# Performance work log

Hardware: AMD Instinct MI355X
Metric: run time of the kernel (lower is better)

The kernel has to match this reference:

```python
import jax, jax.numpy as jnp
import numpy as np

B, S, D, H = 2, 2048, 1024, 16
HD = D // H
NEG = -10000.0


def setup_inputs() -> dict:
    key = jax.random.key(0)
    ks = jax.random.split(key, 9)
    # xavier-uniform-like scale for square d_model x d_model weights
    lim = float(np.sqrt(6.0 / (D + D)))
    mk_w = lambda k: jax.random.uniform(k, (D, D), jnp.float32, -lim, lim)
    return {
        "q": jax.random.normal(ks[0], (B, S, D), jnp.float32),
        "k": jax.random.normal(ks[1], (B, S, D), jnp.float32),
        "v": jax.random.normal(ks[2], (B, S, D), jnp.float32),
        "attn_mask": jax.random.randint(ks[3], (B, S), 0, 2, jnp.int32),
        "Wq": mk_w(ks[4]),
        "Wk": mk_w(ks[5]),
        "Wv": mk_w(ks[6]),
        "Wo": mk_w(ks[7]),
        "mask_future": 1,
    }


def reference(q, k, v, attn_mask, Wq, Wk, Wv, Wo, mask_future):
    # nn.Linear(bias=False): y = x @ W.T
    def split_heads(x, W):
        return (x @ W.T).reshape(B, S, H, HD).transpose(0, 2, 1, 3)  # [B,H,S,HD]

    qh = split_heads(q, Wq)
    kh = split_heads(k, Wk)
    vh = split_heads(v, Wv)

    scale = 1.0 / np.sqrt(HD)
    scores = jnp.einsum("bhld,bhsd->bhls", qh, kh) * scale  # [B,H,L,S]

    if mask_future:  # static python flag
        rows = jnp.arange(S)[:, None]
        cols = jnp.arange(S)[None, :]
        causal_bias = jnp.where(cols > rows, jnp.float32(NEG), jnp.float32(0.0))
        scores = scores + causal_bias

    # masked_fill(attn_mask == 0, -10000): sets score exactly to NEG (after bias add)
    pad = attn_mask[:, None, None, :]  # [B,1,1,S]
    scores = jnp.where(pad == 0, jnp.float32(NEG), scores)

    probs = jax.nn.softmax(scores, axis=-1)
    ctx = jnp.einsum("bhls,bhsd->bhld", probs, vh)  # [B,H,L,HD]
    ctx = ctx.transpose(0, 2, 1, 3).reshape(B, S, D)
    return ctx @ Wo.T
```

## Files before the change

### kernel.cpp

```cpp
#include <hip/hip_runtime.h>
#include <hip/hip_bf16.h>

typedef __attribute__((ext_vector_type(8))) short bf16x8;
typedef __attribute__((ext_vector_type(4))) short bf16x4;
typedef __attribute__((ext_vector_type(4))) float f32x4;

#define B_ 2
#define S_ 2048
#define D_ 1024
#define H_ 16
#define HD_ 64
#define M_ 4096
#define NEGV (-10000.0f)

#if __has_builtin(__builtin_amdgcn_mfma_f32_16x16x16bf16_1k)
#define HAVE_MFMA16 1
#else
#define HAVE_MFMA16 0
#endif

static __device__ __forceinline__ unsigned short f2bf(float x) {
  __hip_bfloat16 h = __float2bfloat16(x);
  return *reinterpret_cast<unsigned short*>(&h);
}

static __device__ __forceinline__ bf16x8 cvt8(const float* p) {
  float4 a = *reinterpret_cast<const float4*>(p);
  float4 b = *reinterpret_cast<const float4*>(p + 4);
  bf16x8 r;
  r[0] = (short)f2bf(a.x); r[1] = (short)f2bf(a.y);
  r[2] = (short)f2bf(a.z); r[3] = (short)f2bf(a.w);
  r[4] = (short)f2bf(b.x); r[5] = (short)f2bf(b.y);
  r[6] = (short)f2bf(b.z); r[7] = (short)f2bf(b.w);
  return r;
}

template<bool AF32, bool BF32, bool HSPLIT>
static __device__ __forceinline__ void gemm_core(const void* Av, const void* Bv,
                                                 unsigned short* Asm, unsigned short* Bsm,
                                                 int m0, int n0, f32x4 (*acc)[4]) {
  constexpr int BK = 64, LDT = 72;
  constexpr int K = 1024;
  const int tid = threadIdx.x;
  const int lane = tid & 63, wid = tid >> 6;
  const int wm = wid >> 1, wn = wid & 1;
  const int l15 = lane & 15, l4 = lane >> 4;

  for (int k0 = 0; k0 < K; k0 += BK) {
    __syncthreads();
#pragma unroll
    for (int i = 0; i < 4; ++i) {
      int idx = tid + 256 * i;
      int row = idx >> 3, k8 = (idx & 7) * 8;
      bf16x8 va, vb;
      if constexpr (AF32) {
        va = cvt8((const float*)Av + (size_t)(m0 + row) * K + k0 + k8);
      } else if constexpr (HSPLIT) {
        const int m = m0 + row, kk = k0 + k8;
        const int bb = m >> 11, s = m & 2047;
        va = *reinterpret_cast<const bf16x8*>(
            (const unsigned short*)Av +
            (((size_t)(bb * H_ + (kk >> 6)) * S_ + s) * HD_ + (kk & 63)));
      } else {
        va = *reinterpret_cast<const bf16x8*>((const unsigned short*)Av + (size_t)(m0 + row) * K + k0 + k8);
      }
      if constexpr (BF32) {
        vb = cvt8((const float*)Bv + (size_t)(n0 + row) * K + k0 + k8);
      } else {
        vb = *reinterpret_cast<const bf16x8*>((const unsigned short*)Bv + (size_t)(n0 + row) * K + k0 + k8);
      }
      *reinterpret_cast<bf16x8*>(&Asm[row * LDT + k8]) = va;
      *reinterpret_cast<bf16x8*>(&Bsm[row * LDT + k8]) = vb;
    }
    __syncthreads();
#pragma unroll
    for (int kk = 0; kk < 2; ++kk) {
      bf16x8 af[4], bfr[4];
#pragma unroll
      for (int f = 0; f < 4; ++f) {
        af[f]  = *reinterpret_cast<const bf16x8*>(&Asm[(wm * 64 + f * 16 + l15) * LDT + kk * 32 + l4 * 8]);
        bfr[f] = *reinterpret_cast<const bf16x8*>(&Bsm[(wn * 64 + f * 16 + l15) * LDT + kk * 32 + l4 * 8]);
      }
#pragma unroll
      for (int fm = 0; fm < 4; ++fm)
#pragma unroll
        for (int fn = 0; fn < 4; ++fn)
          acc[fm][fn] = __builtin_amdgcn_mfma_f32_16x16x32_bf16(af[fm], bfr[fn], acc[fm][fn], 0, 0, 0);
    }
  }
}

__global__ __launch_bounds__(256) void gemm_qkv3(const float* __restrict__ q,
                                                 const float* __restrict__ k,
                                                 const float* __restrict__ v,
                                                 const float* __restrict__ Wq,
                                                 const float* __restrict__ Wk,
                                                 const float* __restrict__ Wv,
                                                 unsigned short* __restrict__ Qh,
                                                 unsigned short* __restrict__ Kh,
                                                 unsigned short* __restrict__ Vt) {
  constexpr int LDT = 72;
  __shared__ unsigned short Asm[128 * LDT];
  __shared__ unsigned short Bsm[128 * LDT];
  const int z = blockIdx.z;
  const float* A  = (z == 0) ? q  : (z == 1) ? k  : v;
  const float* Bw = (z == 0) ? Wq : (z == 1) ? Wk : Wv;
  const int m0 = blockIdx.y * 128, n0 = blockIdx.x * 128;
  const int lane = threadIdx.x & 63, wid = threadIdx.x >> 6;
  const int wm = wid >> 1, wn = wid & 1;
  const int l15 = lane & 15, l4 = lane >> 4;
  f32x4 acc[4][4] = {};
  gemm_core<true, true, false>(A, Bw, Asm, Bsm, m0, n0, acc);

#pragma unroll
  for (int fm = 0; fm < 4; ++fm) {
#pragma unroll
    for (int fn = 0; fn < 4; ++fn) {
      const int mg0 = m0 + wm * 64 + fm * 16 + l4 * 4;
      const int ng  = n0 + wn * 64 + fn * 16 + l15;
      const int bidx = mg0 >> 11, s = mg0 & 2047;
      const int h = ng >> 6, d = ng & 63;
      if (z < 2) {
        unsigned short* C = (z == 0) ? Qh : Kh;
#pragma unroll
        for (int r = 0; r < 4; ++r)
          C[((size_t)((bidx * H_ + h) * S_ + s + r)) * HD_ + d] = f2bf(acc[fm][fn][r]);
      } else {
        ushort4 pk;
        pk.x = f2bf(acc[fm][fn][0]); pk.y = f2bf(acc[fm][fn][1]);
        pk.z = f2bf(acc[fm][fn][2]); pk.w = f2bf(acc[fm][fn][3]);
        *reinterpret_cast<ushort4*>(&Vt[((size_t)((bidx * H_ + h) * HD_ + d)) * S_ + s]) = pk;
      }
    }
  }
}

__global__ __launch_bounds__(256) void gemm_oproj(const void* __restrict__ Av,
                                                  const void* __restrict__ Bv,
                                                  float* __restrict__ Cout) {
  constexpr int LDT = 72;
  __shared__ unsigned short Asm[128 * LDT];
  __shared__ unsigned short Bsm[128 * LDT];
  const int m0 = blockIdx.y * 128, n0 = blockIdx.x * 128;
  const int lane = threadIdx.x & 63, wid = threadIdx.x >> 6;
  const int wm = wid >> 1, wn = wid & 1;
  const int l15 = lane & 15, l4 = lane >> 4;
  f32x4 acc[4][4] = {};
  gemm_core<false, true, true>(Av, Bv, Asm, Bsm, m0, n0, acc);

#pragma unroll
  for (int fm = 0; fm < 4; ++fm)
#pragma unroll
    for (int fn = 0; fn < 4; ++fn) {
      const int mg0 = m0 + wm * 64 + fm * 16 + l4 * 4;
      const int ng  = n0 + wn * 64 + fn * 16 + l15;
#pragma unroll
      for (int r = 0; r < 4; ++r)
        Cout[(size_t)(mg0 + r) * 1024 + ng] = acc[fm][fn][r];
    }
}

__global__ __launch_bounds__(256) void attn_fwd(const unsigned short* Qh,
                                                const unsigned short* __restrict__ Kh,
                                                const unsigned short* __restrict__ Vt,
                                                const int* __restrict__ attn_mask,
                                                const int* __restrict__ mask_future,
                                                unsigned short* ctx) {
  constexpr int KVB = 128;
  constexpr int LDK = 72;
  constexpr int LDV = 136;
  __shared__ unsigned short Ksm[KVB * LDK];
  __shared__ unsigned short Vsm[64 * LDV];
#if !HAVE_MFMA16
  __shared__ unsigned short Psm[4][16 * LDV];
#endif
  __shared__ int s_any;
  const int tid = threadIdx.x, lane = tid & 63, wid = tid >> 6;
  const int l15 = lane & 15, l4 = lane >> 4;
  const int bh = blockIdx.y, b = bh >> 4;
  const int q0 = ((int)(blockIdx.x + blockIdx.y) & 31) * 64;
  const bool causal = (mask_future[0] != 0);

  if (tid == 0) s_any = 0;
  __syncthreads();
  for (int i = tid; i <= q0; i += 256)
    if (attn_mask[b * S_ + i]) s_any = 1;
  __syncthreads();
  const int kb_end = (causal && s_any) ? (q0 + 64) : S_;

  const unsigned short* Qb = Qh + (size_t)bh * S_ * HD_;
  const unsigned short* Kb = Kh + (size_t)bh * S_ * HD_;
  const unsigned short* Vb = Vt + (size_t)bh * HD_ * S_;
  const int* mrow = attn_mask + b * S_;

  const int qrow = q0 + wid * 16 + l15;
  const bf16x8 qf0 = *reinterpret_cast<const bf16x8*>(&Qb[(size_t)qrow * HD_ + l4 * 8]);
  const bf16x8 qf1 = *reinterpret_cast<const bf16x8*>(&Qb[(size_t)qrow * HD_ + 32 + l4 * 8]);

  float m_run = -1e30f, l_run = 0.f;
  f32x4 o[4] = {};

  bf16x8 kreg[4], vreg[4];
#pragma unroll
  for (int j = 0; j < 4; ++j) {
    const int idx = tid + 256 * j;
    kreg[j] = *reinterpret_cast<const bf16x8*>(&Kb[(size_t)(idx >> 3) * HD_ + (idx & 7) * 8]);
    vreg[j] = *reinterpret_cast<const bf16x8*>(&Vb[(size_t)(idx >> 4) * S_ + (idx & 15) * 8]);
  }

  for (int kb = 0; kb < kb_end; kb += KVB) {
    __syncthreads();
#pragma unroll
    for (int j = 0; j < 4; ++j) {
      const int idx = tid + 256 * j;
      *reinterpret_cast<bf16x8*>(&Ksm[(idx >> 3) * LDK + (idx & 7) * 8]) = kreg[j];
      *reinterpret_cast<bf16x8*>(&Vsm[(idx >> 4) * LDV + (idx & 15) * 8]) = vreg[j];
    }
    __syncthreads();

    if (kb + KVB < kb_end) {
      const int kn = kb + KVB;
#pragma unroll
      for (int j = 0; j < 4; ++j) {
        const int idx = tid + 256 * j;
        kreg[j] = *reinterpret_cast<const bf16x8*>(&Kb[(size_t)(kn + (idx >> 3)) * HD_ + (idx & 7) * 8]);
        vreg[j] = *reinterpret_cast<const bf16x8*>(&Vb[(size_t)(idx >> 4) * S_ + kn + (idx & 15) * 8]);
      }
    }

    f32x4 sc[8];
#pragma unroll
    for (int nf = 0; nf < 8; ++nf) {
      bf16x8 kf0 = *reinterpret_cast<const bf16x8*>(&Ksm[(nf * 16 + l15) * LDK + l4 * 8]);
      bf16x8 kf1 = *reinterpret_cast<const bf16x8*>(&Ksm[(nf * 16 + l15) * LDK + 32 + l4 * 8]);
      f32x4 z = {};
      z = __builtin_amdgcn_mfma_f32_16x16x32_bf16(kf0, qf0, z, 0, 0, 0);
      z = __builtin_amdgcn_mfma_f32_16x16x32_bf16(kf1, qf1, z, 0, 0, 0);
      sc[nf] = z;
    }

    float p[8][4];
    float mx = -1e30f;
#pragma unroll
    for (int nf = 0; nf < 8; ++nf) {
      const int4 mk4 = *reinterpret_cast<const int4*>(&mrow[kb + nf * 16 + l4 * 4]);
      const int kbase = kb + nf * 16 + l4 * 4;
#pragma unroll
      for (int r = 0; r < 4; ++r) {
        float vv = sc[nf][r] * 0.125f;
        if (causal && (kbase + r) > qrow) vv += NEGV;
        const int mkr = (r == 0) ? mk4.x : (r == 1) ? mk4.y : (r == 2) ? mk4.z : mk4.w;
        if (mkr == 0) vv = NEGV;
        p[nf][r] = vv;
        mx = fmaxf(mx, vv);
      }
    }
    mx = fmaxf(mx, __shfl_xor(mx, 16));
    mx = fmaxf(mx, __shfl_xor(mx, 32));
    const float m_new = fmaxf(m_run, mx);
    const float scale = __expf(m_run - m_new);
    float s_loc = 0.f;
#pragma unroll
    for (int nf = 0; nf < 8; ++nf)
#pragma unroll
      for (int r = 0; r < 4; ++r) {
        float e = __expf(p[nf][r] - m_new);
        p[nf][r] = e;
        s_loc += e;
      }
    s_loc += __shfl_xor(s_loc, 16);
    s_loc += __shfl_xor(s_loc, 32);
    l_run = l_run * scale + s_loc;
    m_run = m_new;

    float sq[4];
#pragma unroll
    for (int r = 0; r < 4; ++r) sq[r] = __shfl(scale, l4 * 4 + r);
#pragma unroll
    for (int nf2 = 0; nf2 < 4; ++nf2)
#pragma unroll
      for (int r = 0; r < 4; ++r) o[nf2][r] *= sq[r];

#if HAVE_MFMA16
    bf16x4 pk[8];
#pragma unroll
    for (int nf = 0; nf < 8; ++nf) {
      bf16x4 t;
      t[0] = (short)f2bf(p[nf][0]); t[1] = (short)f2bf(p[nf][1]);
      t[2] = (short)f2bf(p[nf][2]); t[3] = (short)f2bf(p[nf][3]);
      pk[nf] = t;
    }
#pragma unroll
    for (int nf2 = 0; nf2 < 4; ++nf2) {
#pragma unroll
      for (int nf = 0; nf < 8; ++nf) {
        bf16x4 vf = *reinterpret_cast<const bf16x4*>(&Vsm[(nf2 * 16 + l15) * LDV + nf * 16 + l4 * 4]);
        o[nf2] = __builtin_amdgcn_mfma_f32_16x16x16bf16_1k(pk[nf], vf, o[nf2], 0, 0, 0);
      }
    }
#else
    unsigned short* Pw = &Psm[wid][0];
#pragma unroll
    for (int nf = 0; nf < 8; ++nf)
#pragma unroll
      for (int r = 0; r < 4; ++r)
        Pw[l15 * LDV + nf * 16 + l4 * 4 + r] = f2bf(p[nf][r]);
#pragma unroll
    for (int nf2 = 0; nf2 < 4; ++nf2) {
#pragma unroll
      for (int kk = 0; kk < 4; ++kk) {
        bf16x8 pf = *reinterpret_cast<const bf16x8*>(&Pw[l15 * LDV + kk * 32 + l4 * 8]);
        bf16x8 vf = *reinterpret_cast<const bf16x8*>(&Vsm[(nf2 * 16 + l15) * LDV + kk * 32 + l4 * 8]);
        o[nf2] = __builtin_amdgcn_mfma_f32_16x16x32_bf16(pf, vf, o[nf2], 0, 0, 0);
      }
    }
#endif
  }

  const float linv = 1.f / l_run;
  float lq[4];
#pragma unroll
  for (int r = 0; r < 4; ++r) lq[r] = __shfl(linv, l4 * 4 + r);
#pragma unroll
  for (int nf2 = 0; nf2 < 4; ++nf2)
#pragma unroll
    for (int r = 0; r < 4; ++r) {
      const int rowg = q0 + wid * 16 + l4 * 4 + r;
      ctx[((size_t)bh * S_ + rowg) * HD_ + nf2 * 16 + l15] = f2bf(o[nf2][r] * lq[r]);
    }
}

extern "C" void kernel_launch(void* const* d_in, const int* in_sizes, int n_in,
                              void* d_out, int out_size, void* d_ws, size_t ws_size,
                              hipStream_t stream) {
  const float* q = (const float*)d_in[0];
  const float* k = (const float*)d_in[1];
  const float* v = (const float*)d_in[2];
  const int* attn_mask = (const int*)d_in[3];
  const float* Wq = (const float*)d_in[4];
  const float* Wk = (const float*)d_in[5];
  const float* Wv = (const float*)d_in[6];
  const float* Wo = (const float*)d_in[7];
  const int* mask_future = (const int*)d_in[8];

  const size_t n16 = (size_t)M_ * D_;
  unsigned short* ws0 = (unsigned short*)d_ws;
  unsigned short* ws1 = ws0 + n16;
  unsigned short* Vt  = (unsigned short*)d_out;
  float* out = (float*)d_out;
  (void)in_sizes; (void)n_in; (void)out_size; (void)ws_size;

  gemm_qkv3<<<dim3(8, 32, 3), 256, 0, stream>>>(q, k, v, Wq, Wk, Wv, ws0, ws1, Vt);
  attn_fwd<<<dim3(S_ / 64, B_ * H_), 256, 0, stream>>>(ws0, ws1, Vt, attn_mask, mask_future, ws0);
  gemm_oproj<<<dim3(8, 32), 256, 0, stream>>>(ws0, Wo, out);
}
```

Before: 203.0 us.

## Pre-convert inputs to bf16 and use direct-to-LDS swizzled GEMM loads

Adds a conversion kernel that turns q, k, v and all weights into bf16 once, so the projection GEMMs stop converting fp32 inside their load loops. New GEMM cores load tiles with global_load_lds into XOR-swizzled LDS and use the 16x16x32 bf16 MFMA. The attention tile order switches to an XOR-based swizzle to balance causal work across heads. The cost is an extra kernel launch and extra workspace traffic for the bf16 copies, and there is a fallback to the old path when the workspace is too small.

```diff
diff --git a/kernel.cpp b/kernel.cpp
--- a/kernel.cpp
+++ b/kernel.cpp
@@ -12,6 +12,9 @@
 #define HD_ 64
 #define M_ 4096
 #define NEGV (-10000.0f)
+
+#define NQ_ 4194304
+#define NW_ 1048576
 
 #if __has_builtin(__builtin_amdgcn_mfma_f32_16x16x16bf16_1k)
 #define HAVE_MFMA16 1
@@ -34,6 +37,155 @@
   r[6] = (short)f2bf(b.z); r[7] = (short)f2bf(b.w);
   return r;
 }
+
+static __device__ __forceinline__ void gl_lds16(const unsigned short* g, unsigned short* l) {
+#if __has_builtin(__builtin_amdgcn_global_load_lds)
+  __builtin_amdgcn_global_load_lds(
+      (const __attribute__((address_space(1))) unsigned int*)g,
+      (__attribute__((address_space(3))) unsigned int*)l, 16, 0, 0);
+#else
+  *reinterpret_cast<bf16x8*>(l) = *reinterpret_cast<const bf16x8*>(g);
+#endif
+}
+
+
+__global__ __launch_bounds__(256) void cvt_all(const float* __restrict__ q,
+                                               const float* __restrict__ k,
+                                               const float* __restrict__ v,
+                                               const float* __restrict__ wq,
+                                               const float* __restrict__ wk,
+                                               const float* __restrict__ wv,
+                                               const float* __restrict__ wo,
+                                               unsigned short* __restrict__ dst) {
+  for (size_t c = (size_t)blockIdx.x * 256 + threadIdx.x; c < 2097152; c += (size_t)2048 * 256) {
+    const size_t e = c * 8;
+    const float* s;
+    if (e < (size_t)NQ_)            s = q  + e;
+    else if (e < (size_t)2 * NQ_)   s = k  + (e - (size_t)NQ_);
+    else if (e < (size_t)3 * NQ_)   s = v  + (e - (size_t)2 * NQ_);
+    else if (e < (size_t)3 * NQ_ + NW_)     s = wq + (e - (size_t)3 * NQ_);
+    else if (e < (size_t)3 * NQ_ + 2 * NW_) s = wk + (e - (size_t)3 * NQ_ - NW_);
+    else if (e < (size_t)3 * NQ_ + 3 * NW_) s = wv + (e - (size_t)3 * NQ_ - 2 * NW_);
+    else                                    s = wo + (e - (size_t)3 * NQ_ - 3 * NW_);
+    *reinterpret_cast<bf16x8*>(dst + e) = cvt8(s);
+  }
+}
+
+template<bool HSPLIT>
+static __device__ __forceinline__ void core_fast(const unsigned short* A,
+                                                 const unsigned short* Bw,
+                                                 unsigned short* Asm, unsigned short* Bsm,
+                                                 int m0, int n0, f32x4 (*acc)[4]) {
+  const int tid = threadIdx.x, lane = tid & 63, wid = tid >> 6;
+  const int wm = wid >> 1, wn = wid & 1;
+  const int l15 = lane & 15, l4 = lane >> 4;
+
+  for (int k0 = 0; k0 < 1024; k0 += 64) {
+    __syncthreads();
+#pragma unroll
+    for (int i = 0; i < 4; ++i) {
+      const int idx = tid + 256 * i;
+      const int row = idx >> 3;
+      const int ce = ((idx & 7) * 8) ^ ((row & 7) << 3);
+      const unsigned short* ga;
+      if constexpr (HSPLIT) {
+        const int m = m0 + row, kk = k0 + ce;
+        const int bb = m >> 11, s = m & 2047;
+        ga = A + (((size_t)(bb * H_ + (kk >> 6)) * S_ + s) * HD_ + (kk & 63));
+      } else {
+        ga = A + (size_t)(m0 + row) * 1024 + k0 + ce;
+      }
+      gl_lds16(ga, Asm + (size_t)idx * 8);
+      gl_lds16(Bw + (size_t)(n0 + row) * 1024 + k0 + ce, Bsm + (size_t)idx * 8);
+    }
+    __syncthreads();
+#pragma unroll
+    for (int kk = 0; kk < 2; ++kk) {
+      bf16x8 af[4], bfr[4];
+#pragma unroll
+      for (int f = 0; f < 4; ++f) {
+        const int ra = wm * 64 + f * 16 + l15;
+        const int ca = (kk * 32 + l4 * 8) ^ ((ra & 7) << 3);
+        af[f] = *reinterpret_cast<const bf16x8*>(&Asm[ra * 64 + ca]);
+        const int rb = wn * 64 + f * 16 + l15;
+        const int cb = (kk * 32 + l4 * 8) ^ ((rb & 7) << 3);
+        bfr[f] = *reinterpret_cast<const bf16x8*>(&Bsm[rb * 64 + cb]);
+      }
+#pragma unroll
+      for (int fm = 0; fm < 4; ++fm)
+#pragma unroll
+        for (int fn = 0; fn < 4; ++fn)
+          acc[fm][fn] = __builtin_amdgcn_mfma_f32_16x16x32_bf16(af[fm], bfr[fn], acc[fm][fn], 0, 0, 0);
+    }
+  }
+}
+
+__global__ __launch_bounds__(256) void gemm_qkv_fast(const unsigned short* __restrict__ qbf,
+                                                     const unsigned short* __restrict__ kbf,
+                                                     const unsigned short* __restrict__ vbf,
+                                                     const unsigned short* __restrict__ wbf,
+                                                     unsigned short* __restrict__ Qh,
+                                                     unsigned short* __restrict__ Kh,
+                                                     unsigned short* __restrict__ Vt) {
+  __shared__ unsigned short Asm[128 * 64];
+  __shared__ unsigned short Bsm[128 * 64];
+  const int z = blockIdx.z;
+  const unsigned short* A  = (z == 0) ? qbf : (z == 1) ? kbf : vbf;
+  const unsigned short* Bw = wbf + (size_t)z * NW_;
+  const int m0 = blockIdx.y * 128, n0 = blockIdx.x * 128;
+  const int lane = threadIdx.x & 63, wid = threadIdx.x >> 6;
+  const int wm = wid >> 1, wn = wid & 1;
+  const int l15 = lane & 15, l4 = lane >> 4;
+  f32x4 acc[4][4] = {};
+  core_fast<false>(A, Bw, Asm, Bsm, m0, n0, acc);
+
+#pragma unroll
+  for (int fm = 0; fm < 4; ++fm) {
+#pragma unroll
+    for (int fn = 0; fn < 4; ++fn) {
+      const int mg0 = m0 + wm * 64 + fm * 16 + l4 * 4;
+      const int ng  = n0 + wn * 64 + fn * 16 + l15;
+      const int bidx = mg0 >> 11, s = mg0 & 2047;
+      const int h = ng >> 6, d = ng & 63;
+      if (z < 2) {
+        unsigned short* C = (z == 0) ? Qh : Kh;
+#pragma unroll
+        for (int r = 0; r < 4; ++r)
+          C[((size_t)((bidx * H_ + h) * S_ + s + r)) * HD_ + d] = f2bf(acc[fm][fn][r]);
+      } else {
+        ushort4 pk;
+        pk.x = f2bf(acc[fm][fn][0]); pk.y = f2bf(acc[fm][fn][1]);
+        pk.z = f2bf(acc[fm][fn][2]); pk.w = f2bf(acc[fm][fn][3]);
+        *reinterpret_cast<ushort4*>(&Vt[((size_t)((bidx * H_ + h) * HD_ + d)) * S_ + s]) = pk;
+      }
+    }
+  }
+}
+
+__global__ __launch_bounds__(256) void gemm_o_fast(const unsigned short* __restrict__ ctx,
+                                                   const unsigned short* __restrict__ wobf,
+                                                   float* __restrict__ Cout) {
+  __shared__ unsigned short Asm[128 * 64];
+  __shared__ unsigned short Bsm[128 * 64];
+  const int m0 = blockIdx.y * 128, n0 = blockIdx.x * 128;
+  const int lane = threadIdx.x & 63, wid = threadIdx.x >> 6;
+  const int wm = wid >> 1, wn = wid & 1;
+  const int l15 = lane & 15, l4 = lane >> 4;
+  f32x4 acc[4][4] = {};
+  core_fast<true>(ctx, wobf, Asm, Bsm, m0, n0, acc);
+
+#pragma unroll
+  for (int fm = 0; fm < 4; ++fm)
+#pragma unroll
+    for (int fn = 0; fn < 4; ++fn) {
+      const int mg0 = m0 + wm * 64 + fm * 16 + l4 * 4;
+      const int ng  = n0 + wn * 64 + fn * 16 + l15;
+#pragma unroll
+      for (int r = 0; r < 4; ++r)
+        Cout[(size_t)(mg0 + r) * 1024 + ng] = acc[fm][fn][r];
+    }
+}
+
 
 template<bool AF32, bool BF32, bool HSPLIT>
 static __device__ __forceinline__ void gemm_core(const void* Av, const void* Bv,
@@ -178,7 +330,8 @@
   const int tid = threadIdx.x, lane = tid & 63, wid = tid >> 6;
   const int l15 = lane & 15, l4 = lane >> 4;
   const int bh = blockIdx.y, b = bh >> 4;
-  const int q0 = ((int)(blockIdx.x + blockIdx.y) & 31) * 64;
+  const int tswz[4] = {0, 31, 16, 15};
+  const int q0 = ((int)(blockIdx.x ^ tswz[(bh >> 3) & 3]) & 31) * 64;
   const bool causal = (mask_future[0] != 0);
 
   if (tid == 0) s_any = 0;
@@ -343,14 +496,32 @@
   const float* Wo = (const float*)d_in[7];
   const int* mask_future = (const int*)d_in[8];
 
-  const size_t n16 = (size_t)M_ * D_;
-  unsigned short* ws0 = (unsigned short*)d_ws;
-  unsigned short* ws1 = ws0 + n16;
-  unsigned short* Vt  = (unsigned short*)d_out;
+  unsigned short* ws = (unsigned short*)d_ws;
+  unsigned short* Vt = (unsigned short*)d_out;
   float* out = (float*)d_out;
-  (void)in_sizes; (void)n_in; (void)out_size; (void)ws_size;
-
-  gemm_qkv3<<<dim3(8, 32, 3), 256, 0, stream>>>(q, k, v, Wq, Wk, Wv, ws0, ws1, Vt);
-  attn_fwd<<<dim3(S_ / 64, B_ * H_), 256, 0, stream>>>(ws0, ws1, Vt, attn_mask, mask_future, ws0);
-  gemm_oproj<<<dim3(8, 32), 256, 0, stream>>>(ws0, Wo, out);
-}
+  (void)in_sizes; (void)n_in; (void)out_size;
+
+  const size_t CVT_ELEMS = (size_t)3 * NQ_ + 4 * NW_;
+  const size_t NEED = (CVT_ELEMS + 2 * (size_t)NQ_) * 2;
+
+  if (ws_size >= NEED) {
+    unsigned short* cvt = ws;
+    unsigned short* qbf = cvt;
+    unsigned short* kbf = cvt + (size_t)NQ_;
+    unsigned short* vbf = cvt + (size_t)2 * NQ_;
+    unsigned short* wbf = cvt + (size_t)3 * NQ_;
+    unsigned short* Qh  = cvt + CVT_ELEMS;
+    unsigned short* Kh  = Qh + (size_t)NQ_;
+
+    cvt_all<<<2048, 256, 0, stream>>>(q, k, v, Wq, Wk, Wv, Wo, cvt);
+    gemm_qkv_fast<<<dim3(8, 32, 3), 256, 0, stream>>>(qbf, kbf, vbf, wbf, Qh, Kh, Vt);
+    attn_fwd<<<dim3(32, 32), 256, 0, stream>>>(Qh, Kh, Vt, attn_mask, mask_future, Qh);
+    gemm_o_fast<<<dim3(8, 32), 256, 0, stream>>>(Qh, wbf + (size_t)3 * NW_, out);
+  } else {
+    unsigned short* Qh = ws;
+    unsigned short* Kh = ws + (size_t)NQ_;
+    gemm_qkv3<<<dim3(8, 32, 3), 256, 0, stream>>>(q, k, v, Wq, Wk, Wv, Qh, Kh, Vt);
+    attn_fwd<<<dim3(32, 32), 256, 0, stream>>>(Qh, Kh, Vt, attn_mask, mask_future, Qh);
+    gemm_oproj<<<dim3(8, 32), 256, 0, stream>>>(Qh, Wo, out);
+  }
+}
```

Result: faster. 181.0 us (-10.8%).
